# Kernel tuning notes

Hardware: AMD Instinct MI355X
Metric: run time of the kernel (lower is better)

## Reference

```python
import jax, jax.numpy as jnp
import numpy as np

# Sizes: B graphs of N nodes each, K nearest neighbours, D=feat_dim=nhid, C=pos_dim
B, N, K, D, C = 4, 1024, 128, 32, 2
L = 3                     # number of EGNN conv layers
E_IN = 2 * D + 1          # edge MLP input: feats_i | feats_j | rel_dist (edge_dim=0, fourier=0)
E_H = 2 * E_IN            # edge MLP hidden


def _lin(key, fan_in, fan_out):
    kw, kb = jax.random.split(key)
    w = jax.random.normal(kw, (fan_in, fan_out), jnp.float32) / np.sqrt(fan_in)
    b = jax.random.normal(kb, (fan_out,), jnp.float32) * 0.01
    return w, b


def _stack(key, fan_in, fan_out):
    ws, bs = zip(*[_lin(k, fan_in, fan_out) for k in jax.random.split(key, L)])
    return jnp.stack(ws), jnp.stack(bs)


def setup_inputs() -> dict:
    key = jax.random.key(0)
    ks = jax.random.split(key, 10)
    feat_ = jax.random.normal(ks[0], (B * N, D), jnp.float32)
    coor_ = jax.random.normal(ks[1], (B * N, C), jnp.float32)
    batch = jnp.full((B,), N, dtype=jnp.int32)   # per-graph node counts (equal-size graphs)
    embed_w, embed_b = _lin(ks[2], D, D)         # embed: Linear(feat_dim, nhid)
    e1_w, e1_b = _stack(ks[3], E_IN, E_H)        # edge MLP
    e2_w, e2_b = _stack(ks[4], E_H, D)           # -> m_dim = nhid
    gate_w, gate_b = _stack(ks[5], D, 1)         # soft_edges gate
    c1_w, c1_b = _stack(ks[6], D, 4 * D)         # coors MLP
    c2_w, c2_b = _stack(ks[7], 4 * D, 1)
    n1_w, n1_b = _stack(ks[8], 2 * D, 2 * D)     # node MLP
    n2_w, n2_b = _stack(ks[9], 2 * D, D)
    coors_scale = jnp.full((L, 1), 1e-2, jnp.float32)  # CoorsNorm scale (init 1e-2)
    return dict(feat_=feat_, coor_=coor_, batch=batch, embed_w=embed_w, embed_b=embed_b,
                e1_w=e1_w, e1_b=e1_b, e2_w=e2_w, e2_b=e2_b, gate_w=gate_w, gate_b=gate_b,
                c1_w=c1_w, c1_b=c1_b, c2_w=c2_w, c2_b=c2_b, n1_w=n1_w, n1_b=n1_b,
                n2_w=n2_w, n2_b=n2_b, coors_scale=coors_scale)


def _lrelu(x):
    return jax.nn.leaky_relu(x, 0.1)


def _gather(x, idx):
    # x: [B, n, d], idx: [B, n, k] -> [B, n, k, d]
    return jax.vmap(lambda xb, ib: xb[ib])(x, idx)


def _egnn_layer(feats, coors, p):
    (e1_w, e1_b, e2_w, e2_b, gate_w, gate_b, c1_w, c1_b, c2_w, c2_b,
     n1_w, n1_b, n2_w, n2_b, scale) = p
    # pairwise squared distances; k smallest (self included, valid_radius=inf)
    diff = coors[:, :, None, :] - coors[:, None, :, :]      # [B,n,n,C]
    dist = jnp.sum(diff * diff, axis=-1)                    # [B,n,n]
    neg_d, idx = jax.lax.top_k(-dist, K)                    # k nearest
    rel_dist = -neg_d[..., None]                            # [B,n,K,1]
    rel_coors = coors[:, :, None, :] - _gather(coors, idx)  # [B,n,K,C]
    feats_j = _gather(feats, idx)                           # [B,n,K,D]
    feats_i = jnp.broadcast_to(feats[:, :, None, :], feats_j.shape)
    edge_in = jnp.concatenate([feats_i, feats_j, rel_dist], axis=-1)  # [B,n,K,E_IN]
    # edge MLP: Lin -> act -> Lin -> act ; soft edge gate
    m = _lrelu(_lrelu(edge_in @ e1_w + e1_b) @ e2_w + e2_b)            # [B,n,K,D]
    m = m * jax.nn.sigmoid(m @ gate_w + gate_b)
    # coordinate update: coors_mlp -> scalar weights; CoorsNorm on rel coords
    cw = (_lrelu(m @ c1_w + c1_b) @ c2_w + c2_b)[..., 0]               # [B,n,K]
    norm = jnp.maximum(jnp.linalg.norm(rel_coors, axis=-1, keepdims=True), 1e-8)
    rel_n = rel_coors / norm * scale
    coors_out = jnp.einsum('bik,bikc->bic', cw, rel_n) + coors
    # feature update: sum-pool messages, node MLP with residual
    m_i = jnp.sum(m, axis=2)                                           # [B,n,D]
    node_in = jnp.concatenate([feats, m_i], axis=-1)
    feats_out = _lrelu(node_in @ n1_w + n1_b) @ n2_w + n2_b + feats
    return feats_out, coors_out


def reference(feat_, coor_, batch, embed_w, embed_b, e1_w, e1_b, e2_w, e2_b,
              gate_w, gate_b, c1_w, c1_b, c2_w, c2_b, n1_w, n1_b, n2_w, n2_b,
              coors_scale):
    # embed MLP (dropout is identity at p=0 / eval), then batch equal-size graphs
    feats = _lrelu(feat_ @ embed_w + embed_b).reshape(B, N, D)
    coors = coor_.reshape(B, N, C)
    for l in range(L):
        p = (e1_w[l], e1_b[l], e2_w[l], e2_b[l], gate_w[l], gate_b[l],
             c1_w[l], c1_b[l], c2_w[l], c2_b[l], n1_w[l], n1_b[l],
             n2_w[l], n2_b[l], coors_scale[l])
        feats, coors = _egnn_layer(feats, coors, p)
    return feats.reshape(B * N, D)
```

## Files before the change

### kernel.cpp

```cpp
#include <hip/hip_runtime.h>
#include <hip/hip_bf16.h>
#include <math.h>

#define BB 4
#define NN 1024
#define KK 128
#define DD 32
#define LL 3
#define EH 130

typedef float f32x4 __attribute__((ext_vector_type(4)));
typedef short s16x8 __attribute__((ext_vector_type(8)));

__device__ __forceinline__ float lrelu(float x) { return fmaxf(x, 0.1f * x); }

__device__ __forceinline__ unsigned pk2(float a, float b) {
    __hip_bfloat162 h = __float22bfloat162_rn(float2{a, b});
    return *(unsigned*)&h;
}
__device__ __forceinline__ unsigned short bf16_hu(float v) {
    return (unsigned short)((__float_as_uint(v) + 0x8000u) >> 16);
}
__device__ __forceinline__ unsigned short bf16_rne(float v) {
    unsigned u = __float_as_uint(v);
    return (unsigned short)((u + 0x7fffu + ((u >> 16) & 1u)) >> 16);
}
__device__ __forceinline__ float bf2f(unsigned short h) {
    return __uint_as_float(((unsigned)h) << 16);
}

__device__ __forceinline__ void knn_block(const float2* __restrict__ cbp, int i, int t,
                                          unsigned* __restrict__ hist,
                                          volatile unsigned* __restrict__ scr,
                                          int* __restrict__ nb) {
    const int lane = t & 63, wid = t >> 6;
    unsigned* histw = hist + wid * 256;
    const float2 ci = cbp[i];
    unsigned k[4];
#pragma unroll
    for (int s = 0; s < 4; s++) {
        float2 cj = cbp[wid * 256 + s * 64 + lane];
        float dx = ci.x - cj.x, dy = ci.y - cj.y;
        float d = __fadd_rn(__fmul_rn(dx, dx), __fmul_rn(dy, dy));
        k[s] = __float_as_uint(d);
    }
    unsigned prefix = 0u;
    unsigned r = KK - 1;
#pragma unroll
    for (int pass = 0; pass < 4; pass++) {
        const int sh = 24 - 8 * pass;
        const unsigned mpref = (pass == 0) ? 0u : (0xFFFFFFFFu << (sh + 8));
        ((uint4*)histw)[lane] = uint4{0u, 0u, 0u, 0u};
#pragma unroll
        for (int s = 0; s < 4; s++) {
            if ((k[s] & mpref) == prefix)
                atomicAdd(&histw[(k[s] >> sh) & 255u], 1u);
        }
        __syncthreads();
        unsigned tot = hist[t] + hist[256 + t] + hist[512 + t] + hist[768 + t];
        unsigned incl = tot;
#pragma unroll
        for (int off = 1; off < 64; off <<= 1) {
            unsigned v = __shfl_up(incl, off, 64);
            if (lane >= off) incl += v;
        }
        if (lane == 63) scr[wid] = incl;
        __syncthreads();
        unsigned woff = 0;
#pragma unroll
        for (int w = 0; w < 4; w++)
            if (w < wid) woff += scr[w];
        incl += woff;
        const unsigned excl = incl - tot;
        if (r >= excl && r < incl) { scr[4] = (unsigned)t; scr[5] = r - excl; }
        __syncthreads();
        prefix |= scr[4] << sh;
        r = scr[5];
    }
    const unsigned dstar = prefix;

    const unsigned long long below = (1ull << lane) - 1ull;
    unsigned long long mL[4], mE[4];
    unsigned cntL = 0, cntE = 0;
#pragma unroll
    for (int s = 0; s < 4; s++) {
        mL[s] = __ballot(k[s] < dstar);
        mE[s] = __ballot(k[s] == dstar);
        cntL += (unsigned)__popcll(mL[s]);
        cntE += (unsigned)__popcll(mE[s]);
    }
    if (lane == 0) { scr[8 + wid] = cntL; scr[12 + wid] = cntE; }
    __syncthreads();
    unsigned offL = 0, offE = 0, totalL = 0;
#pragma unroll
    for (int w = 0; w < 4; w++) {
        unsigned cl = scr[8 + w];
        if (w < wid) { offL += cl; offE += scr[12 + w]; }
        totalL += cl;
    }
    unsigned run = offL;
#pragma unroll
    for (int s = 0; s < 4; s++) {
        if (k[s] < dstar) nb[run + (unsigned)__popcll(mL[s] & below)] = wid * 256 + s * 64 + lane;
        run += (unsigned)__popcll(mL[s]);
    }
    const int need = KK - (int)totalL;
    unsigned tie = offE;
#pragma unroll
    for (int s = 0; s < 4; s++) {
        if (k[s] == dstar) {
            unsigned r2 = tie + (unsigned)__popcll(mE[s] & below);
            if ((int)r2 < need) nb[totalL + r2] = wid * 256 + s * 64 + lane;
        }
        tie += (unsigned)__popcll(mE[s]);
    }
}

__global__ __launch_bounds__(128) void prep_kernel(
    const float* __restrict__ feat,
    const float* __restrict__ ew, const float* __restrict__ eb,
    float* __restrict__ fout, unsigned short* __restrict__ fouth, unsigned short* __restrict__ foutl,
    const float* __restrict__ e1w,
    const float* __restrict__ e2w, const float* __restrict__ e2b,
    const float* __restrict__ c1w,
    unsigned short* __restrict__ e2f, unsigned short* __restrict__ c1f,
    unsigned short* __restrict__ e1Jh, unsigned short* __restrict__ e1Jl) {
    const int bid = blockIdx.x;
    const int t = threadIdx.x;
    if (bid < 2048) {
        const int n0 = bid * 2;
        if (t < 64) {
            const int nl = t >> 5, o = t & 31;
            const float* f = feat + (size_t)(n0 + nl) * DD;
            float a = eb[o];
#pragma unroll
            for (int k = 0; k < DD; k++) a = fmaf(f[k], ew[k * DD + o], a);
            a = lrelu(a);
            const size_t off = (size_t)(n0 + nl) * DD + o;
            fout[off] = a;
            const unsigned short h = bf16_rne(a);
            fouth[off] = h;
            foutl[off] = bf16_rne(a - bf2f(h));
        }
    } else {
        const int A_ = LL * 5120;
        const int B_ = A_ + LL * 4096;
        const int C_ = B_ + LL * 4608;
        const int TOT = C_ + LL * 4608;
        for (int u = (bid - 2048) * 128 + t; u < TOT; u += 432 * 128) {
            if (u < A_) {
                int l = u / 5120, v = u - l * 5120;
                int jj = v & 7, la = (v >> 3) & 63, nt = (v >> 9) & 1, c = v >> 10;
                int n = nt * 16 + (la & 15);
                float val;
                if (c < 4) {
                    int k = 32 * c + (la >> 4) * 8 + jj;
                    val = e2w[(size_t)l * EH * DD + k * DD + n];
                } else {
                    int ks = (la >> 4) * 8 + jj;
                    val = (ks == 0) ? e2w[((size_t)l * EH + 128) * DD + n]
                        : (ks == 1) ? e2w[((size_t)l * EH + 129) * DD + n]
                        : (ks == 2) ? e2b[(size_t)l * DD + n] : 0.f;
                }
                e2f[u] = bf16_rne(val);
            } else if (u < B_) {
                int v = u - A_;
                int jj = v & 7, la = (v >> 3) & 63, nt = (v >> 9) & 7, l = v >> 12;
                int k = (la >> 4) * 8 + jj;
                int n = nt * 16 + (la & 15);
                c1f[v] = bf16_rne(c1w[(size_t)l * DD * 128 + k * 128 + n]);
            } else {
                const int isLo = (u >= C_);
                int v = u - (isLo ? C_ : B_);
                int l = v / 4608, w = v - l * 4608;
                int jj = w & 7, la = (w >> 3) & 63, nt = w >> 9;
                int col = nt * 16 + (la & 15);
                int k = (la >> 4) * 8 + jj;
                float val = (col < EH) ? e1w[(size_t)l * 65 * EH + (size_t)(DD + k) * EH + col] : 0.f;
                const unsigned short h = bf16_rne(val);
                if (!isLo) e1Jh[v] = h;
                else       e1Jl[v] = bf16_rne(val - bf2f(h));
            }
        }
    }
}

__global__ __launch_bounds__(256) void layer_kernel(
    const float* __restrict__ feats_in,
    const unsigned short* __restrict__ finh, const unsigned short* __restrict__ finl,
    const float* __restrict__ coors_in,
    const float* __restrict__ e1wI,
    const float* __restrict__ e1b_l,
    const float* __restrict__ w65,
    const unsigned short* __restrict__ e2f,
    const unsigned short* __restrict__ c1f,
    const unsigned short* __restrict__ e1Jh, const unsigned short* __restrict__ e1Jl,
    const float* __restrict__ gw, const float* __restrict__ gb,
    const float* __restrict__ c1b, const float* __restrict__ c2w, const float* __restrict__ c2b,
    const float* __restrict__ n1w, const float* __restrict__ n1b,
    const float* __restrict__ n2w, const float* __restrict__ n2b,
    const float* __restrict__ scale,
    float* __restrict__ feats_out,
    unsigned short* __restrict__ fouth, unsigned short* __restrict__ foutl,
    float* __restrict__ coors_out) {
    const int node = blockIdx.x;
    const int b = node >> 10;
    const int t = threadIdx.x;
    const int lane = t & 63, wid = t >> 6;
    const int ln = lane & 15, q = lane >> 4;
    const int rowbase = wid * 32;

    __shared__ __align__(16) float shi[144];
    __shared__ __align__(16) float sw65[144];
    __shared__ __align__(16) unsigned short smA[4 * 32 * 32];
    __shared__ unsigned sknn[16];
    __shared__ float sx0[128], sx1[128], su[128], sv[128], srd[128];
    __shared__ int snb[128];
    __shared__ float sgw[DD], sfi[DD];
    __shared__ float sc1b[128], sc2w[128];
    __shared__ float redm[4][DD], redc[4][2];
    __shared__ float sni[2 * DD], shd[2 * DD];
    __shared__ float sp1[4][2 * DD], sp2[4][DD];

    for (int u = t; u < 144; u += 256) sw65[u] = (u < EH) ? w65[u] : 0.f;
    if (t < DD) { sfi[t] = feats_in[node * DD + t]; sgw[t] = gw[t]; }
    if (t >= 128 && t < 256) { sc1b[t - 128] = c1b[t - 128]; sc2w[t - 128] = c2w[t - 128]; }
    __syncthreads();

    if (t < EH) {
        float a = e1b_l[t];
#pragma unroll
        for (int k = 0; k < DD; k++) a = fmaf(sfi[k], e1wI[k * EH + t], a);
        shi[t] = a;
    } else if (t < 144) {
        shi[t] = 0.f;
    }

    knn_block((const float2*)coors_in + (size_t)b * NN, node & (NN - 1), t,
              (unsigned*)smA, sknn, snb);
    __syncthreads();

    const float cix = coors_in[node * 2], ciy = coors_in[node * 2 + 1];
    if (t < 128) {
        const int j = snb[t];
        const float2 cj = *(const float2*)(coors_in + ((size_t)(b * NN) + j) * 2);
        const float dx = cix - cj.x, dy = ciy - cj.y;
        const float rd = __fadd_rn(__fmul_rn(dx, dx), __fmul_rn(dy, dy));
        srd[t] = rd;
        const float nrm = fmaxf(sqrtf(rd), 1e-8f);
        const float s = scale[0] / nrm;
        su[t] = dx * s;
        sv[t] = dy * s;
    }
    __syncthreads();

    s16x8 ah[2], al[2];
    float rd8[2][4];
#pragma unroll
    for (int mt = 0; mt < 2; mt++) {
        const int row = rowbase + mt * 16 + ln;
        const size_t jb = ((size_t)(b * NN) + snb[row]) * DD;
        ah[mt] = *(const s16x8*)(finh + jb + q * 8);
        al[mt] = *(const s16x8*)(finl + jb + q * 8);
#pragma unroll
        for (int r = 0; r < 4; r++) rd8[mt][r] = srd[rowbase + mt * 16 + q * 4 + r];
    }

    const f32x4 zz = {0.f, 0.f, 0.f, 0.f};
    f32x4 accA[2][2];
    accA[0][0] = zz; accA[0][1] = zz; accA[1][0] = zz; accA[1][1] = zz;
    unsigned short* smw = smA + wid * (32 * 32);

#pragma unroll 1
    for (int c = 0; c < 4; c++) {
        s16x8 bh0 = *(const s16x8*)(e1Jh + ((c * 2 + 0) * 64 + lane) * 8);
        s16x8 bl0 = *(const s16x8*)(e1Jl + ((c * 2 + 0) * 64 + lane) * 8);
        s16x8 bh1 = *(const s16x8*)(e1Jh + ((c * 2 + 1) * 64 + lane) * 8);
        s16x8 bl1 = *(const s16x8*)(e1Jl + ((c * 2 + 1) * 64 + lane) * 8);
        const float h0 = shi[c * 32 + ln],      h1 = shi[c * 32 + 16 + ln];
        const float w0 = sw65[c * 32 + ln],     w1 = sw65[c * 32 + 16 + ln];
        const f32x4 ci0 = {h0, h0, h0, h0};
        const f32x4 ci1 = {h1, h1, h1, h1};
#pragma unroll
        for (int mt = 0; mt < 2; mt++) {
            f32x4 s0 = __builtin_amdgcn_mfma_f32_16x16x32_bf16(ah[mt], bh0, ci0, 0, 0, 0);
            s0 = __builtin_amdgcn_mfma_f32_16x16x32_bf16(ah[mt], bl0, s0, 0, 0, 0);
            s0 = __builtin_amdgcn_mfma_f32_16x16x32_bf16(al[mt], bh0, s0, 0, 0, 0);
            f32x4 s1 = __builtin_amdgcn_mfma_f32_16x16x32_bf16(ah[mt], bh1, ci1, 0, 0, 0);
            s1 = __builtin_amdgcn_mfma_f32_16x16x32_bf16(ah[mt], bl1, s1, 0, 0, 0);
            s1 = __builtin_amdgcn_mfma_f32_16x16x32_bf16(al[mt], bh1, s1, 0, 0, 0);
#pragma unroll
            for (int r = 0; r < 4; r++) {
                const float x0 = lrelu(fmaf(rd8[mt][r], w0, s0[r]));
                const float x1 = lrelu(fmaf(rd8[mt][r], w1, s1[r]));
                const int prow = (r << 3) | (4 * mt + q);
                smw[prow * 32 + ln] = bf16_hu(x0);
                smw[prow * 32 + 16 + ln] = bf16_hu(x1);
            }
        }
        s16x8 b0 = *(const s16x8*)(e2f + ((c * 2 + 0) * 64 + lane) * 8);
        s16x8 b1 = *(const s16x8*)(e2f + ((c * 2 + 1) * 64 + lane) * 8);
#pragma unroll
        for (int mt = 0; mt < 2; mt++) {
            const int prow = ((ln & 3) << 3) | (4 * mt + (ln >> 2));
            s16x8 a4x = *(const s16x8*)(smw + prow * 32 + q * 8);
            accA[mt][0] = __builtin_amdgcn_mfma_f32_16x16x32_bf16(a4x, b0, accA[mt][0], 0, 0, 0);
            accA[mt][1] = __builtin_amdgcn_mfma_f32_16x16x32_bf16(a4x, b1, accA[mt][1], 0, 0, 0);
        }
    }

    {
        s16x8 bh8 = *(const s16x8*)(e1Jh + (8 * 64 + lane) * 8);
        s16x8 bl8 = *(const s16x8*)(e1Jl + (8 * 64 + lane) * 8);
        const float h8 = shi[128 + ln];
        const float w8 = sw65[128 + ln];
        const f32x4 ci8 = {h8, h8, h8, h8};
#pragma unroll
        for (int mt = 0; mt < 2; mt++) {
            f32x4 s = __builtin_amdgcn_mfma_f32_16x16x32_bf16(ah[mt], bh8, ci8, 0, 0, 0);
            s = __builtin_amdgcn_mfma_f32_16x16x32_bf16(ah[mt], bl8, s, 0, 0, 0);
            s = __builtin_amdgcn_mfma_f32_16x16x32_bf16(al[mt], bh8, s, 0, 0, 0);
#pragma unroll
            for (int r = 0; r < 4; r++) {
                const float v = lrelu(fmaf(rd8[mt][r], w8, s[r]));
                const int row = rowbase + mt * 16 + q * 4 + r;
                if (ln == 0) sx0[row] = v;
                else if (ln == 1) sx1[row] = v;
            }
        }
    }

    {
        s16x8 b40 = *(const s16x8*)(e2f + (8 * 64 + lane) * 8);
        s16x8 b41 = *(const s16x8*)(e2f + (9 * 64 + lane) * 8);
#pragma unroll
        for (int mt = 0; mt < 2; mt++) {
            const int row = rowbase + mt * 16 + ln;
            union { s16x8 v; unsigned u[4]; } A;
            const unsigned p0 = pk2(sx0[row], sx1[row]);
            A.u[0] = (q == 0) ? p0 : 0u;
            A.u[1] = (q == 0) ? 0x00003f80u : 0u;
            A.u[2] = 0u;
            A.u[3] = 0u;
            accA[mt][0] = __builtin_amdgcn_mfma_f32_16x16x32_bf16(A.v, b40, accA[mt][0], 0, 0, 0);
            accA[mt][1] = __builtin_amdgcn_mfma_f32_16x16x32_bf16(A.v, b41, accA[mt][1], 0, 0, 0);
        }
    }

    s16x8 cfr[8];
#pragma unroll
    for (int g8 = 0; g8 < 8; g8++)
        cfr[g8] = *(const s16x8*)(c1f + (g8 * 64 + lane) * 8);

#pragma unroll
    for (int mt = 0; mt < 2; mt++)
#pragma unroll
        for (int nt = 0; nt < 2; nt++)
#pragma unroll
            for (int r = 0; r < 4; r++)
                accA[mt][nt][r] = lrelu(accA[mt][nt][r]);

    const float gbv = gb[0];
#pragma unroll
    for (int mt = 0; mt < 2; mt++) {
        float p[4];
#pragma unroll
        for (int r = 0; r < 4; r++)
            p[r] = accA[mt][0][r] * sgw[ln] + accA[mt][1][r] * sgw[16 + ln];
#pragma unroll
        for (int off = 1; off <= 8; off <<= 1)
#pragma unroll
            for (int r = 0; r < 4; r++) p[r] += __shfl_xor(p[r], off);
#pragma unroll
        for (int r = 0; r < 4; r++) {
            const float g = 1.f / (1.f + __expf(-(p[r] + gbv)));
            accA[mt][0][r] *= g;
            accA[mt][1][r] *= g;
        }
    }

    float mi0 = 0.f, mi1 = 0.f;
#pragma unroll
    for (int mt = 0; mt < 2; mt++)
#pragma unroll
        for (int r = 0; r < 4; r++) { mi0 += accA[mt][0][r]; mi1 += accA[mt][1][r]; }
    mi0 += __shfl_xor(mi0, 16); mi0 += __shfl_xor(mi0, 32);
    mi1 += __shfl_xor(mi1, 16); mi1 += __shfl_xor(mi1, 32);
    if (lane < 16) { redm[wid][lane] = mi0; redm[wid][16 + lane] = mi1; }

#pragma unroll
    for (int mt = 0; mt < 2; mt++)
#pragma unroll
        for (int nt = 0; nt < 2; nt++)
#pragma unroll
            for (int r = 0; r < 4; r++) {
                const int prow = (r << 3) | (4 * mt + q);
                smw[prow * 32 + nt * 16 + ln] = bf16_hu(accA[mt][nt][r]);
            }

    s16x8 a4[2];
#pragma unroll
    for (int mt = 0; mt < 2; mt++) {
        const int prow = ((ln & 3) << 3) | (4 * mt + (ln >> 2));
        a4[mt] = *(const s16x8*)(smw + prow * 32 + q * 8);
    }

    float cacc[2][4];
#pragma unroll
    for (int mt = 0; mt < 2; mt++)
#pragma unroll
        for (int r = 0; r < 4; r++) cacc[mt][r] = 0.f;

#pragma unroll
    for (int g = 0; g < 4; g++) {
        const float cb0 = sc1b[(2 * g + 0) * 16 + ln];
        const float cb1 = sc1b[(2 * g + 1) * 16 + ln];
        const f32x4 ci0 = {cb0, cb0, cb0, cb0};
        const f32x4 ci1 = {cb1, cb1, cb1, cb1};
        f32x4 c20[2], c21[2];
#pragma unroll
        for (int mt = 0; mt < 2; mt++) {
            c20[mt] = __builtin_amdgcn_mfma_f32_16x16x32_bf16(a4[mt], cfr[2 * g + 0], ci0, 0, 0, 0);
            c21[mt] = __builtin_amdgcn_mfma_f32_16x16x32_bf16(a4[mt], cfr[2 * g + 1], ci1, 0, 0, 0);
        }
#pragma unroll
        for (int h = 0; h < 2; h++) {
            const float c2wv = sc2w[(2 * g + h) * 16 + ln];
#pragma unroll
            for (int mt = 0; mt < 2; mt++)
#pragma unroll
                for (int r = 0; r < 4; r++) {
                    const float v = (h ? c21[mt][r] : c20[mt][r]);
                    cacc[mt][r] = fmaf(lrelu(v), c2wv, cacc[mt][r]);
                }
        }
    }
#pragma unroll
    for (int off = 1; off <= 8; off <<= 1)
#pragma unroll
        for (int mt = 0; mt < 2; mt++)
#pragma unroll
            for (int r = 0; r < 4; r++) cacc[mt][r] += __shfl_xor(cacc[mt][r], off);

    const float c2bv = c2b[0];
    float vxp = 0.f, vyp = 0.f;
    if (ln == 0) {
#pragma unroll
        for (int mt = 0; mt < 2; mt++)
#pragma unroll
            for (int r = 0; r < 4; r++) {
                const int row = rowbase + mt * 16 + q * 4 + r;
                const float cw = cacc[mt][r] + c2bv;
                vxp = fmaf(cw, su[row], vxp);
                vyp = fmaf(cw, sv[row], vyp);
            }
    }
    vxp += __shfl_xor(vxp, 16); vxp += __shfl_xor(vxp, 32);
    vyp += __shfl_xor(vyp, 16); vyp += __shfl_xor(vyp, 32);
    if (lane == 0) { redc[wid][0] = vxp; redc[wid][1] = vyp; }

    __syncthreads();
    if (t < DD) {
        sni[t] = sfi[t];
        sni[DD + t] = redm[0][t] + redm[1][t] + redm[2][t] + redm[3][t];
    }
    __syncthreads();
    {
        const int o = t & 63, p = t >> 6;
        float a = 0.f;
#pragma unroll
        for (int k = 0; k < 16; k++) a = fmaf(sni[p * 16 + k], n1w[(p * 16 + k) * 64 + o], a);
        sp1[p][o] = a;
    }
    __syncthreads();
    if (t < 2 * DD)
        shd[t] = lrelu(n1b[t] + ((sp1[0][t] + sp1[1][t]) + (sp1[2][t] + sp1[3][t])));
    __syncthreads();
    if (t < 128) {
        const int o = t & 31, p = t >> 5;
        float a = 0.f;
#pragma unroll
        for (int k = 0; k < 16; k++) a = fmaf(shd[p * 16 + k], n2w[(p * 16 + k) * DD + o], a);
        sp2[p][o] = a;
    }
    __syncthreads();
    if (t < DD) {
        const float val = n2b[t] + ((sp2[0][t] + sp2[1][t]) + (sp2[2][t] + sp2[3][t])) + sfi[t];
        feats_out[node * DD + t] = val;
        if (fouth) {
            const unsigned short h = bf16_rne(val);
            fouth[node * DD + t] = h;
            foutl[node * DD + t] = bf16_rne(val - bf2f(h));
        }
    }
    if (t == 0) {
        coors_out[node * 2]     = cix + redc[0][0] + redc[1][0] + redc[2][0] + redc[3][0];
        coors_out[node * 2 + 1] = ciy + redc[0][1] + redc[1][1] + redc[2][1] + redc[3][1];
    }
}

extern "C" void kernel_launch(void* const* d_in, const int* in_sizes, int n_in,
                              void* d_out, int out_size, void* d_ws, size_t ws_size,
                              hipStream_t stream) {
    const float* feat_   = (const float*)d_in[0];
    const float* coor_   = (const float*)d_in[1];
    const float* embed_w = (const float*)d_in[3];
    const float* embed_b = (const float*)d_in[4];
    const float* e1_w    = (const float*)d_in[5];
    const float* e1_b    = (const float*)d_in[6];
    const float* e2_w    = (const float*)d_in[7];
    const float* e2_b    = (const float*)d_in[8];
    const float* gate_w  = (const float*)d_in[9];
    const float* gate_b  = (const float*)d_in[10];
    const float* c1_w    = (const float*)d_in[11];
    const float* c1_b    = (const float*)d_in[12];
    const float* c2_w    = (const float*)d_in[13];
    const float* c2_b    = (const float*)d_in[14];
    const float* n1_w    = (const float*)d_in[15];
    const float* n1_b    = (const float*)d_in[16];
    const float* n2_w    = (const float*)d_in[17];
    const float* n2_b    = (const float*)d_in[18];
    const float* cscale  = (const float*)d_in[19];

    float* ws = (float*)d_ws;
    float* fa   = ws;   ws += BB * NN * DD;
    float* fb   = ws;   ws += BB * NN * DD;
    float* ca   = ws;   ws += BB * NN * 2;
    float* cb2  = ws;   ws += BB * NN * 2;
    unsigned short* e2f  = (unsigned short*)ws;
    unsigned short* c1f  = e2f + LL * 5120;
    unsigned short* e1Jh = c1f + LL * 4096;
    unsigned short* e1Jl = e1Jh + LL * 4608;
    unsigned short* fah  = e1Jl + LL * 4608;
    unsigned short* fal  = fah + BB * NN * DD;
    unsigned short* fbh  = fal + BB * NN * DD;
    unsigned short* fbl  = fbh + BB * NN * DD;

    prep_kernel<<<2048 + 432, 128, 0, stream>>>(feat_, embed_w, embed_b,
                                                fa, fah, fal,
                                                e1_w, e2_w, e2_b, c1_w,
                                                e2f, c1f, e1Jh, e1Jl);

    const float* fin = fa;
    const unsigned short* finh = fah;
    const unsigned short* finl = fal;
    const float* cin = coor_;
    float* fouts[LL]          = {fb, fa, (float*)d_out};
    unsigned short* fouth[LL] = {fbh, fah, nullptr};
    unsigned short* foutl[LL] = {fbl, fal, nullptr};
    float* couts[LL] = {ca, cb2, ca};

    for (int l = 0; l < LL; l++) {
        layer_kernel<<<BB * NN, 256, 0, stream>>>(
            fin, finh, finl, cin,
            e1_w + (size_t)l * 65 * EH,
            e1_b + (size_t)l * EH,
            e1_w + ((size_t)l * 65 + 64) * EH,
            e2f + (size_t)l * 5120,
            c1f + (size_t)l * 4096,
            e1Jh + (size_t)l * 4608,
            e1Jl + (size_t)l * 4608,
            gate_w + (size_t)l * DD,
            gate_b + l,
            c1_b + (size_t)l * 128,
            c2_w + (size_t)l * 128,
            c2_b + l,
            n1_w + (size_t)l * 64 * 64,
            n1_b + (size_t)l * 64,
            n2_w + (size_t)l * 64 * 32,
            n2_b + (size_t)l * DD,
            cscale + l,
            fouts[l], fouth[l], foutl[l],
            couts[l]);
        fin = fouts[l];
        finh = fouth[l];
        finl = foutl[l];
        cin = couts[l];
    }
}
```

Before: 322.4 us.

## Process two nodes per block with joint radix-select kNN

```diff
diff --git a/kernel.cpp b/kernel.cpp
--- a/kernel.cpp
+++ b/kernel.cpp
@@ -8,6 +8,7 @@
 #define DD 32
 #define LL 3
 #define EH 130
+#define SMS 40
 
 typedef float f32x4 __attribute__((ext_vector_type(4)));
 typedef short s16x8 __attribute__((ext_vector_type(8)));
@@ -29,91 +30,111 @@
     return __uint_as_float(((unsigned)h) << 16);
 }
 
-__device__ __forceinline__ void knn_block(const float2* __restrict__ cbp, int i, int t,
-                                          unsigned* __restrict__ hist,
-                                          volatile unsigned* __restrict__ scr,
-                                          int* __restrict__ nb) {
+__device__ __forceinline__ void knn2_block(const float2* __restrict__ cbp, int iA, int iB,
+                                           int t,
+                                           unsigned* __restrict__ hist,
+                                           volatile unsigned* __restrict__ scr,
+                                           int* __restrict__ nbA, int* __restrict__ nbB) {
     const int lane = t & 63, wid = t >> 6;
-    unsigned* histw = hist + wid * 256;
-    const float2 ci = cbp[i];
-    unsigned k[4];
+    unsigned* hA = hist + wid * 256;
+    unsigned* hB = hist + 1024 + wid * 256;
+    const float2 cA = cbp[iA], cB = cbp[iB];
+    unsigned kA[4], kB[4];
 #pragma unroll
     for (int s = 0; s < 4; s++) {
         float2 cj = cbp[wid * 256 + s * 64 + lane];
-        float dx = ci.x - cj.x, dy = ci.y - cj.y;
-        float d = __fadd_rn(__fmul_rn(dx, dx), __fmul_rn(dy, dy));
-        k[s] = __float_as_uint(d);
-    }
-    unsigned prefix = 0u;
-    unsigned r = KK - 1;
+        float dxA = cA.x - cj.x, dyA = cA.y - cj.y;
+        kA[s] = __float_as_uint(__fadd_rn(__fmul_rn(dxA, dxA), __fmul_rn(dyA, dyA)));
+        float dxB = cB.x - cj.x, dyB = cB.y - cj.y;
+        kB[s] = __float_as_uint(__fadd_rn(__fmul_rn(dxB, dxB), __fmul_rn(dyB, dyB)));
+    }
+    unsigned prefA = 0u, rA = KK - 1, prefB = 0u, rB = KK - 1;
 #pragma unroll
     for (int pass = 0; pass < 4; pass++) {
         const int sh = 24 - 8 * pass;
         const unsigned mpref = (pass == 0) ? 0u : (0xFFFFFFFFu << (sh + 8));
-        ((uint4*)histw)[lane] = uint4{0u, 0u, 0u, 0u};
+        ((uint4*)hA)[lane] = uint4{0u, 0u, 0u, 0u};
+        ((uint4*)hB)[lane] = uint4{0u, 0u, 0u, 0u};
 #pragma unroll
         for (int s = 0; s < 4; s++) {
-            if ((k[s] & mpref) == prefix)
-                atomicAdd(&histw[(k[s] >> sh) & 255u], 1u);
-        }
-        __syncthreads();
-        unsigned tot = hist[t] + hist[256 + t] + hist[512 + t] + hist[768 + t];
-        unsigned incl = tot;
+            if ((kA[s] & mpref) == prefA) atomicAdd(&hA[(kA[s] >> sh) & 255u], 1u);
+            if ((kB[s] & mpref) == prefB) atomicAdd(&hB[(kB[s] >> sh) & 255u], 1u);
+        }
+        __syncthreads();
+        unsigned totA = hist[t] + hist[256 + t] + hist[512 + t] + hist[768 + t];
+        unsigned totB = hist[1024 + t] + hist[1280 + t] + hist[1536 + t] + hist[1792 + t];
+        unsigned inA = totA, inB = totB;
 #pragma unroll
         for (int off = 1; off < 64; off <<= 1) {
-            unsigned v = __shfl_up(incl, off, 64);
-            if (lane >= off) incl += v;
-        }
-        if (lane == 63) scr[wid] = incl;
-        __syncthreads();
-        unsigned woff = 0;
+            unsigned vA = __shfl_up(inA, off, 64);
+            unsigned vB = __shfl_up(inB, off, 64);
+            if (lane >= off) { inA += vA; inB += vB; }
+        }
+        if (lane == 63) { scr[wid] = inA; scr[4 + wid] = inB; }
+        __syncthreads();
+        unsigned woA = 0, woB = 0;
 #pragma unroll
         for (int w = 0; w < 4; w++)
-            if (w < wid) woff += scr[w];
-        incl += woff;
-        const unsigned excl = incl - tot;
-        if (r >= excl && r < incl) { scr[4] = (unsigned)t; scr[5] = r - excl; }
-        __syncthreads();
-        prefix |= scr[4] << sh;
-        r = scr[5];
-    }
-    const unsigned dstar = prefix;
+            if (w < wid) { woA += scr[w]; woB += scr[4 + w]; }
+        inA += woA; inB += woB;
+        const unsigned exA = inA - totA, exB = inB - totB;
+        if (rA >= exA && rA < inA) { scr[8] = (unsigned)t; scr[9] = rA - exA; }
+        if (rB >= exB && rB < inB) { scr[10] = (unsigned)t; scr[11] = rB - exB; }
+        __syncthreads();
+        prefA |= scr[8] << sh;   rA = scr[9];
+        prefB |= scr[10] << sh;  rB = scr[11];
+    }
+    const unsigned dsA = prefA, dsB = prefB;
 
     const unsigned long long below = (1ull << lane) - 1ull;
-    unsigned long long mL[4], mE[4];
-    unsigned cntL = 0, cntE = 0;
+    unsigned long long mLA[4], mEA[4], mLB[4], mEB[4];
+    unsigned cLA = 0, cEA = 0, cLB = 0, cEB = 0;
 #pragma unroll
     for (int s = 0; s < 4; s++) {
-        mL[s] = __ballot(k[s] < dstar);
-        mE[s] = __ballot(k[s] == dstar);
-        cntL += (unsigned)__popcll(mL[s]);
-        cntE += (unsigned)__popcll(mE[s]);
-    }
-    if (lane == 0) { scr[8 + wid] = cntL; scr[12 + wid] = cntE; }
+        mLA[s] = __ballot(kA[s] < dsA);   mEA[s] = __ballot(kA[s] == dsA);
+        cLA += (unsigned)__popcll(mLA[s]); cEA += (unsigned)__popcll(mEA[s]);
+        mLB[s] = __ballot(kB[s] < dsB);   mEB[s] = __ballot(kB[s] == dsB);
+        cLB += (unsigned)__popcll(mLB[s]); cEB += (unsigned)__popcll(mEB[s]);
+    }
+    if (lane == 0) {
+        scr[12 + wid] = cLA; scr[16 + wid] = cEA;
+        scr[20 + wid] = cLB; scr[24 + wid] = cEB;
+    }
     __syncthreads();
-    unsigned offL = 0, offE = 0, totalL = 0;
+    unsigned offLA = 0, offEA = 0, totLA = 0;
+    unsigned offLB = 0, offEB = 0, totLB = 0;
 #pragma unroll
     for (int w = 0; w < 4; w++) {
-        unsigned cl = scr[8 + w];
-        if (w < wid) { offL += cl; offE += scr[12 + w]; }
-        totalL += cl;
-    }
-    unsigned run = offL;
+        unsigned a = scr[12 + w], bb2 = scr[20 + w];
+        if (w < wid) { offLA += a; offEA += scr[16 + w]; offLB += bb2; offEB += scr[24 + w]; }
+        totLA += a; totLB += bb2;
+    }
+    unsigned runA = offLA, runB = offLB;
 #pragma unroll
     for (int s = 0; s < 4; s++) {
-        if (k[s] < dstar) nb[run + (unsigned)__popcll(mL[s] & below)] = wid * 256 + s * 64 + lane;
-        run += (unsigned)__popcll(mL[s]);
-    }
-    const int need = KK - (int)totalL;
-    unsigned tie = offE;
+        const int cand = wid * 256 + s * 64 + lane;
+        if (kA[s] < dsA) nbA[runA + (unsigned)__popcll(mLA[s] & below)] = cand;
+        runA += (unsigned)__popcll(mLA[s]);
+        if (kB[s] < dsB) nbB[runB + (unsigned)__popcll(mLB[s] & below)] = cand;
+        runB += (unsigned)__popcll(mLB[s]);
+    }
+    const int needA = KK - (int)totLA, needB = KK - (int)totLB;
+    unsigned tieA = offEA, tieB = offEB;
 #pragma unroll
     for (int s = 0; s < 4; s++) {
-        if (k[s] == dstar) {
-            unsigned r2 = tie + (unsigned)__popcll(mE[s] & below);
-            if ((int)r2 < need) nb[totalL + r2] = wid * 256 + s * 64 + lane;
-        }
-        tie += (unsigned)__popcll(mE[s]);
-    }
+        const int cand = wid * 256 + s * 64 + lane;
+        if (kA[s] == dsA) {
+            unsigned r2 = tieA + (unsigned)__popcll(mEA[s] & below);
+            if ((int)r2 < needA) nbA[totLA + r2] = cand;
+        }
+        tieA += (unsigned)__popcll(mEA[s]);
+        if (kB[s] == dsB) {
+            unsigned r2 = tieB + (unsigned)__popcll(mEB[s] & below);
+            if ((int)r2 < needB) nbB[totLB + r2] = cand;
+        }
+        tieB += (unsigned)__popcll(mEB[s]);
+    }
+    __syncthreads();
 }
 
 __global__ __launch_bounds__(128) void prep_kernel(
@@ -203,8 +224,8 @@
     float* __restrict__ feats_out,
     unsigned short* __restrict__ fouth, unsigned short* __restrict__ foutl,
     float* __restrict__ coors_out) {
-    const int node = blockIdx.x;
-    const int b = node >> 10;
+    const int node0 = blockIdx.x * 2;
+    const int b = node0 >> 10;
     const int t = threadIdx.x;
     const int lane = t & 63, wid = t >> 6;
     const int ln = lane & 15, q = lane >> 4;
@@ -212,10 +233,10 @@
 
     __shared__ __align__(16) float shi[144];
     __shared__ __align__(16) float sw65[144];
-    __shared__ __align__(16) unsigned short smA[4 * 32 * 32];
-    __shared__ unsigned sknn[16];
+    __shared__ __align__(16) unsigned short smA[4 * 32 * SMS];
+    __shared__ unsigned sknn[32];
     __shared__ float sx0[128], sx1[128], su[128], sv[128], srd[128];
-    __shared__ int snb[128];
+    __shared__ int snb[2 * 128];
     __shared__ float sgw[DD], sfi[DD];
     __shared__ float sc1b[128], sc2w[128];
     __shared__ float redm[4][DD], redc[4][2];
@@ -223,279 +244,287 @@
     __shared__ float sp1[4][2 * DD], sp2[4][DD];
 
     for (int u = t; u < 144; u += 256) sw65[u] = (u < EH) ? w65[u] : 0.f;
-    if (t < DD) { sfi[t] = feats_in[node * DD + t]; sgw[t] = gw[t]; }
-    if (t >= 128 && t < 256) { sc1b[t - 128] = c1b[t - 128]; sc2w[t - 128] = c2w[t - 128]; }
-    __syncthreads();
-
-    if (t < EH) {
-        float a = e1b_l[t];
-#pragma unroll
-        for (int k = 0; k < DD; k++) a = fmaf(sfi[k], e1wI[k * EH + t], a);
-        shi[t] = a;
-    } else if (t < 144) {
-        shi[t] = 0.f;
-    }
-
-    knn_block((const float2*)coors_in + (size_t)b * NN, node & (NN - 1), t,
-              (unsigned*)smA, sknn, snb);
-    __syncthreads();
-
-    const float cix = coors_in[node * 2], ciy = coors_in[node * 2 + 1];
-    if (t < 128) {
-        const int j = snb[t];
-        const float2 cj = *(const float2*)(coors_in + ((size_t)(b * NN) + j) * 2);
-        const float dx = cix - cj.x, dy = ciy - cj.y;
-        const float rd = __fadd_rn(__fmul_rn(dx, dx), __fmul_rn(dy, dy));
-        srd[t] = rd;
-        const float nrm = fmaxf(sqrtf(rd), 1e-8f);
-        const float s = scale[0] / nrm;
-        su[t] = dx * s;
-        sv[t] = dy * s;
-    }
-    __syncthreads();
-
-    s16x8 ah[2], al[2];
-    float rd8[2][4];
-#pragma unroll
-    for (int mt = 0; mt < 2; mt++) {
-        const int row = rowbase + mt * 16 + ln;
-        const size_t jb = ((size_t)(b * NN) + snb[row]) * DD;
-        ah[mt] = *(const s16x8*)(finh + jb + q * 8);
-        al[mt] = *(const s16x8*)(finl + jb + q * 8);
-#pragma unroll
-        for (int r = 0; r < 4; r++) rd8[mt][r] = srd[rowbase + mt * 16 + q * 4 + r];
-    }
-
+    if (t < DD) sgw[t] = gw[t];
+    if (t >= 128) { sc1b[t - 128] = c1b[t - 128]; sc2w[t - 128] = c2w[t - 128]; }
+
+    knn2_block((const float2*)coors_in + (size_t)b * NN, node0 & (NN - 1),
+               (node0 & (NN - 1)) + 1, t, (unsigned*)smA, sknn, snb, snb + 128);
+
+    unsigned short* smw = smA + wid * (32 * SMS);
     const f32x4 zz = {0.f, 0.f, 0.f, 0.f};
-    f32x4 accA[2][2];
-    accA[0][0] = zz; accA[0][1] = zz; accA[1][0] = zz; accA[1][1] = zz;
-    unsigned short* smw = smA + wid * (32 * 32);
 
 #pragma unroll 1
-    for (int c = 0; c < 4; c++) {
-        s16x8 bh0 = *(const s16x8*)(e1Jh + ((c * 2 + 0) * 64 + lane) * 8);
-        s16x8 bl0 = *(const s16x8*)(e1Jl + ((c * 2 + 0) * 64 + lane) * 8);
-        s16x8 bh1 = *(const s16x8*)(e1Jh + ((c * 2 + 1) * 64 + lane) * 8);
-        s16x8 bl1 = *(const s16x8*)(e1Jl + ((c * 2 + 1) * 64 + lane) * 8);
-        const float h0 = shi[c * 32 + ln],      h1 = shi[c * 32 + 16 + ln];
-        const float w0 = sw65[c * 32 + ln],     w1 = sw65[c * 32 + 16 + ln];
-        const f32x4 ci0 = {h0, h0, h0, h0};
-        const f32x4 ci1 = {h1, h1, h1, h1};
+    for (int nn = 0; nn < 2; nn++) {
+        const int node = node0 + nn;
+        const int* snbn = snb + nn * 128;
+
+        __syncthreads();
+        if (t < DD) sfi[t] = feats_in[node * DD + t];
+        __syncthreads();
+
+        const float cix = coors_in[node * 2], ciy = coors_in[node * 2 + 1];
+        if (t < EH) {
+            float a = e1b_l[t];
+#pragma unroll
+            for (int k = 0; k < DD; k++) a = fmaf(sfi[k], e1wI[k * EH + t], a);
+            shi[t] = a;
+        } else if (t < 144) {
+            shi[t] = 0.f;
+        }
+        if (t < 128) {
+            const int j = snbn[t];
+            const float2 cj = *(const float2*)(coors_in + ((size_t)(b * NN) + j) * 2);
+            const float dx = cix - cj.x, dy = ciy - cj.y;
+            const float rd = __fadd_rn(__fmul_rn(dx, dx), __fmul_rn(dy, dy));
+            srd[t] = rd;
+            const float nrm = fmaxf(sqrtf(rd), 1e-8f);
+            const float s = scale[0] / nrm;
+            su[t] = dx * s;
+            sv[t] = dy * s;
+        }
+        __syncthreads();
+
+        s16x8 ah[2], al[2];
+        float rd8[2][4];
 #pragma unroll
         for (int mt = 0; mt < 2; mt++) {
-            f32x4 s0 = __builtin_amdgcn_mfma_f32_16x16x32_bf16(ah[mt], bh0, ci0, 0, 0, 0);
-            s0 = __builtin_amdgcn_mfma_f32_16x16x32_bf16(ah[mt], bl0, s0, 0, 0, 0);
-            s0 = __builtin_amdgcn_mfma_f32_16x16x32_bf16(al[mt], bh0, s0, 0, 0, 0);
-            f32x4 s1 = __builtin_amdgcn_mfma_f32_16x16x32_bf16(ah[mt], bh1, ci1, 0, 0, 0);
-            s1 = __builtin_amdgcn_mfma_f32_16x16x32_bf16(ah[mt], bl1, s1, 0, 0, 0);
-            s1 = __builtin_amdgcn_mfma_f32_16x16x32_bf16(al[mt], bh1, s1, 0, 0, 0);
+            const int row = rowbase + mt * 16 + ln;
+            const size_t jb = ((size_t)(b * NN) + snbn[row]) * DD;
+            ah[mt] = *(const s16x8*)(finh + jb + q * 8);
+            al[mt] = *(const s16x8*)(finl + jb + q * 8);
+#pragma unroll
+            for (int r = 0; r < 4; r++) rd8[mt][r] = srd[rowbase + mt * 16 + q * 4 + r];
+        }
+
+        f32x4 accA[2][2];
+        accA[0][0] = zz; accA[0][1] = zz; accA[1][0] = zz; accA[1][1] = zz;
+
+#pragma unroll 1
+        for (int c = 0; c < 4; c++) {
+            s16x8 bh0 = *(const s16x8*)(e1Jh + ((c * 2 + 0) * 64 + lane) * 8);
+            s16x8 bl0 = *(const s16x8*)(e1Jl + ((c * 2 + 0) * 64 + lane) * 8);
+            s16x8 bh1 = *(const s16x8*)(e1Jh + ((c * 2 + 1) * 64 + lane) * 8);
+            s16x8 bl1 = *(const s16x8*)(e1Jl + ((c * 2 + 1) * 64 + lane) * 8);
+            const float h0 = shi[c * 32 + ln],      h1 = shi[c * 32 + 16 + ln];
+            const float w0 = sw65[c * 32 + ln],     w1 = sw65[c * 32 + 16 + ln];
+            const f32x4 ci0 = {h0, h0, h0, h0};
+            const f32x4 ci1 = {h1, h1, h1, h1};
+#pragma unroll
+            for (int mt = 0; mt < 2; mt++) {
+                f32x4 s0 = __builtin_amdgcn_mfma_f32_16x16x32_bf16(ah[mt], bh0, ci0, 0, 0, 0);
+                s0 = __builtin_amdgcn_mfma_f32_16x16x32_bf16(ah[mt], bl0, s0, 0, 0, 0);
+                s0 = __builtin_amdgcn_mfma_f32_16x16x32_bf16(al[mt], bh0, s0, 0, 0, 0);
+                f32x4 s1 = __builtin_amdgcn_mfma_f32_16x16x32_bf16(ah[mt], bh1, ci1, 0, 0, 0);
+                s1 = __builtin_amdgcn_mfma_f32_16x16x32_bf16(ah[mt], bl1, s1, 0, 0, 0);
+                s1 = __builtin_amdgcn_mfma_f32_16x16x32_bf16(al[mt], bh1, s1, 0, 0, 0);
+#pragma unroll
+                for (int r = 0; r < 4; r++) {
+                    const float x0 = lrelu(fmaf(rd8[mt][r], w0, s0[r]));
+                    const float x1 = lrelu(fmaf(rd8[mt][r], w1, s1[r]));
+                    const int prow = (r << 3) | (4 * mt + q);
+                    smw[prow * SMS + ln] = bf16_hu(x0);
+                    smw[prow * SMS + 16 + ln] = bf16_hu(x1);
+                }
+            }
+            s16x8 b0 = *(const s16x8*)(e2f + ((c * 2 + 0) * 64 + lane) * 8);
+            s16x8 b1 = *(const s16x8*)(e2f + ((c * 2 + 1) * 64 + lane) * 8);
+#pragma unroll
+            for (int mt = 0; mt < 2; mt++) {
+                const int prow = ((ln & 3) << 3) | (4 * mt + (ln >> 2));
+                s16x8 a4x = *(const s16x8*)(smw + prow * SMS + q * 8);
+                accA[mt][0] = __builtin_amdgcn_mfma_f32_16x16x32_bf16(a4x, b0, accA[mt][0], 0, 0, 0);
+                accA[mt][1] = __builtin_amdgcn_mfma_f32_16x16x32_bf16(a4x, b1, accA[mt][1], 0, 0, 0);
+            }
+        }
+
+        {
+            s16x8 bh8 = *(const s16x8*)(e1Jh + (8 * 64 + lane) * 8);
+            s16x8 bl8 = *(const s16x8*)(e1Jl + (8 * 64 + lane) * 8);
+            const float h8 = shi[128 + ln];
+            const float w8 = sw65[128 + ln];
+            const f32x4 ci8 = {h8, h8, h8, h8};
+#pragma unroll
+            for (int mt = 0; mt < 2; mt++) {
+                f32x4 s = __builtin_amdgcn_mfma_f32_16x16x32_bf16(ah[mt], bh8, ci8, 0, 0, 0);
+                s = __builtin_amdgcn_mfma_f32_16x16x32_bf16(ah[mt], bl8, s, 0, 0, 0);
+                s = __builtin_amdgcn_mfma_f32_16x16x32_bf16(al[mt], bh8, s, 0, 0, 0);
+#pragma unroll
+                for (int r = 0; r < 4; r++) {
+                    const float v = lrelu(fmaf(rd8[mt][r], w8, s[r]));
+                    const int row = rowbase + mt * 16 + q * 4 + r;
+                    if (ln == 0) sx0[row] = v;
+                    else if (ln == 1) sx1[row] = v;
+                }
+            }
+        }
+
+        {
+            s16x8 b40 = *(const s16x8*)(e2f + (8 * 64 + lane) * 8);
+            s16x8 b41 = *(const s16x8*)(e2f + (9 * 64 + lane) * 8);
+#pragma unroll
+            for (int mt = 0; mt < 2; mt++) {
+                const int row = rowbase + mt * 16 + ln;
+                union { s16x8 v; unsigned u[4]; } A;
+                const unsigned p0 = pk2(sx0[row], sx1[row]);
+                A.u[0] = (q == 0) ? p0 : 0u;
+                A.u[1] = (q == 0) ? 0x00003f80u : 0u;
+                A.u[2] = 0u;
+                A.u[3] = 0u;
+                accA[mt][0] = __builtin_amdgcn_mfma_f32_16x16x32_bf16(A.v, b40, accA[mt][0], 0, 0, 0);
+                accA[mt][1] = __builtin_amdgcn_mfma_f32_16x16x32_bf16(A.v, b41, accA[mt][1], 0, 0, 0);
+            }
+        }
+
+        s16x8 cfr[8];
+#pragma unroll
+        for (int g8 = 0; g8 < 8; g8++)
+            cfr[g8] = *(const s16x8*)(c1f + (g8 * 64 + lane) * 8);
+
+#pragma unroll
+        for (int mt = 0; mt < 2; mt++)
+#pragma unroll
+            for (int nt = 0; nt < 2; nt++)
+#pragma unroll
+                for (int r = 0; r < 4; r++)
+                    accA[mt][nt][r] = lrelu(accA[mt][nt][r]);
+
+        const float gbv = gb[0];
+#pragma unroll
+        for (int mt = 0; mt < 2; mt++) {
+            float p[4];
+#pragma unroll
+            for (int r = 0; r < 4; r++)
+                p[r] = accA[mt][0][r] * sgw[ln] + accA[mt][1][r] * sgw[16 + ln];
+#pragma unroll
+            for (int off = 1; off <= 8; off <<= 1)
+#pragma unroll
+                for (int r = 0; r < 4; r++) p[r] += __shfl_xor(p[r], off);
 #pragma unroll
             for (int r = 0; r < 4; r++) {
-                const float x0 = lrelu(fmaf(rd8[mt][r], w0, s0[r]));
-                const float x1 = lrelu(fmaf(rd8[mt][r], w1, s1[r]));
-                const int prow = (r << 3) | (4 * mt + q);
-                smw[prow * 32 + ln] = bf16_hu(x0);
-                smw[prow * 32 + 16 + ln] = bf16_hu(x1);
-            }
-        }
-        s16x8 b0 = *(const s16x8*)(e2f + ((c * 2 + 0) * 64 + lane) * 8);
-        s16x8 b1 = *(const s16x8*)(e2f + ((c * 2 + 1) * 64 + lane) * 8);
+                const float g = 1.f / (1.f + __expf(-(p[r] + gbv)));
+                accA[mt][0][r] *= g;
+                accA[mt][1][r] *= g;
+            }
+        }
+
+        float mi0 = 0.f, mi1 = 0.f;
+#pragma unroll
+        for (int mt = 0; mt < 2; mt++)
+#pragma unroll
+            for (int r = 0; r < 4; r++) { mi0 += accA[mt][0][r]; mi1 += accA[mt][1][r]; }
+        mi0 += __shfl_xor(mi0, 16); mi0 += __shfl_xor(mi0, 32);
+        mi1 += __shfl_xor(mi1, 16); mi1 += __shfl_xor(mi1, 32);
+        if (lane < 16) { redm[wid][lane] = mi0; redm[wid][16 + lane] = mi1; }
+
+#pragma unroll
+        for (int mt = 0; mt < 2; mt++)
+#pragma unroll
+            for (int nt = 0; nt < 2; nt++)
+#pragma unroll
+                for (int r = 0; r < 4; r++) {
+                    const int prow = (r << 3) | (4 * mt + q);
+                    smw[prow * SMS + nt * 16 + ln] = bf16_hu(accA[mt][nt][r]);
+                }
+
+        s16x8 a4[2];
 #pragma unroll
         for (int mt = 0; mt < 2; mt++) {
             const int prow = ((ln & 3) << 3) | (4 * mt + (ln >> 2));
-            s16x8 a4x = *(const s16x8*)(smw + prow * 32 + q * 8);
-            accA[mt][0] = __builtin_amdgcn_mfma_f32_16x16x32_bf16(a4x, b0, accA[mt][0], 0, 0, 0);
-            accA[mt][1] = __builtin_amdgcn_mfma_f32_16x16x32_bf16(a4x, b1, accA[mt][1], 0, 0, 0);
-        }
-    }
-
-    {
-        s16x8 bh8 = *(const s16x8*)(e1Jh + (8 * 64 + lane) * 8);
-        s16x8 bl8 = *(const s16x8*)(e1Jl + (8 * 64 + lane) * 8);
-        const float h8 = shi[128 + ln];
-        const float w8 = sw65[128 + ln];
-        const f32x4 ci8 = {h8, h8, h8, h8};
-#pragma unroll
-        for (int mt = 0; mt < 2; mt++) {
-            f32x4 s = __builtin_amdgcn_mfma_f32_16x16x32_bf16(ah[mt], bh8, ci8, 0, 0, 0);
-            s = __builtin_amdgcn_mfma_f32_16x16x32_bf16(ah[mt], bl8, s, 0, 0, 0);
-            s = __builtin_amdgcn_mfma_f32_16x16x32_bf16(al[mt], bh8, s, 0, 0, 0);
-#pragma unroll
-            for (int r = 0; r < 4; r++) {
-                const float v = lrelu(fmaf(rd8[mt][r], w8, s[r]));
-                const int row = rowbase + mt * 16 + q * 4 + r;
-                if (ln == 0) sx0[row] = v;
-                else if (ln == 1) sx1[row] = v;
-            }
-        }
-    }
-
-    {
-        s16x8 b40 = *(const s16x8*)(e2f + (8 * 64 + lane) * 8);
-        s16x8 b41 = *(const s16x8*)(e2f + (9 * 64 + lane) * 8);
-#pragma unroll
-        for (int mt = 0; mt < 2; mt++) {
-            const int row = rowbase + mt * 16 + ln;
-            union { s16x8 v; unsigned u[4]; } A;
-            const unsigned p0 = pk2(sx0[row], sx1[row]);
-            A.u[0] = (q == 0) ? p0 : 0u;
-            A.u[1] = (q == 0) ? 0x00003f80u : 0u;
-            A.u[2] = 0u;
-            A.u[3] = 0u;
-            accA[mt][0] = __builtin_amdgcn_mfma_f32_16x16x32_bf16(A.v, b40, accA[mt][0], 0, 0, 0);
-            accA[mt][1] = __builtin_amdgcn_mfma_f32_16x16x32_bf16(A.v, b41, accA[mt][1], 0, 0, 0);
-        }
-    }
-
-    s16x8 cfr[8];
-#pragma unroll
-    for (int g8 = 0; g8 < 8; g8++)
-        cfr[g8] = *(const s16x8*)(c1f + (g8 * 64 + lane) * 8);
-
-#pragma unroll
-    for (int mt = 0; mt < 2; mt++)
-#pragma unroll
-        for (int nt = 0; nt < 2; nt++)
-#pragma unroll
-            for (int r = 0; r < 4; r++)
-                accA[mt][nt][r] = lrelu(accA[mt][nt][r]);
-
-    const float gbv = gb[0];
-#pragma unroll
-    for (int mt = 0; mt < 2; mt++) {
-        float p[4];
-#pragma unroll
-        for (int r = 0; r < 4; r++)
-            p[r] = accA[mt][0][r] * sgw[ln] + accA[mt][1][r] * sgw[16 + ln];
+            a4[mt] = *(const s16x8*)(smw + prow * SMS + q * 8);
+        }
+
+        float cacc[2][4];
+#pragma unroll
+        for (int mt = 0; mt < 2; mt++)
+#pragma unroll
+            for (int r = 0; r < 4; r++) cacc[mt][r] = 0.f;
+
+#pragma unroll
+        for (int g = 0; g < 4; g++) {
+            const float cb0 = sc1b[(2 * g + 0) * 16 + ln];
+            const float cb1 = sc1b[(2 * g + 1) * 16 + ln];
+            const f32x4 ci0 = {cb0, cb0, cb0, cb0};
+            const f32x4 ci1 = {cb1, cb1, cb1, cb1};
+            f32x4 c20[2], c21[2];
+#pragma unroll
+            for (int mt = 0; mt < 2; mt++) {
+                c20[mt] = __builtin_amdgcn_mfma_f32_16x16x32_bf16(a4[mt], cfr[2 * g + 0], ci0, 0, 0, 0);
+                c21[mt] = __builtin_amdgcn_mfma_f32_16x16x32_bf16(a4[mt], cfr[2 * g + 1], ci1, 0, 0, 0);
+            }
+#pragma unroll
+            for (int h = 0; h < 2; h++) {
+                const float c2wv = sc2w[(2 * g + h) * 16 + ln];
+#pragma unroll
+                for (int mt = 0; mt < 2; mt++)
+#pragma unroll
+                    for (int r = 0; r < 4; r++) {
+                        const float v = (h ? c21[mt][r] : c20[mt][r]);
+                        cacc[mt][r] = fmaf(lrelu(v), c2wv, cacc[mt][r]);
+                    }
+            }
+        }
 #pragma unroll
         for (int off = 1; off <= 8; off <<= 1)
 #pragma unroll
-            for (int r = 0; r < 4; r++) p[r] += __shfl_xor(p[r], off);
-#pragma unroll
-        for (int r = 0; r < 4; r++) {
-            const float g = 1.f / (1.f + __expf(-(p[r] + gbv)));
-            accA[mt][0][r] *= g;
-            accA[mt][1][r] *= g;
-        }
-    }
-
-    float mi0 = 0.f, mi1 = 0.f;
-#pragma unroll
-    for (int mt = 0; mt < 2; mt++)
-#pragma unroll
-        for (int r = 0; r < 4; r++) { mi0 += accA[mt][0][r]; mi1 += accA[mt][1][r]; }
-    mi0 += __shfl_xor(mi0, 16); mi0 += __shfl_xor(mi0, 32);
-    mi1 += __shfl_xor(mi1, 16); mi1 += __shfl_xor(mi1, 32);
-    if (lane < 16) { redm[wid][lane] = mi0; redm[wid][16 + lane] = mi1; }
-
-#pragma unroll
-    for (int mt = 0; mt < 2; mt++)
-#pragma unroll
-        for (int nt = 0; nt < 2; nt++)
-#pragma unroll
-            for (int r = 0; r < 4; r++) {
-                const int prow = (r << 3) | (4 * mt + q);
-                smw[prow * 32 + nt * 16 + ln] = bf16_hu(accA[mt][nt][r]);
-            }
-
-    s16x8 a4[2];
-#pragma unroll
-    for (int mt = 0; mt < 2; mt++) {
-        const int prow = ((ln & 3) << 3) | (4 * mt + (ln >> 2));
-        a4[mt] = *(const s16x8*)(smw + prow * 32 + q * 8);
-    }
-
-    float cacc[2][4];
-#pragma unroll
-    for (int mt = 0; mt < 2; mt++)
-#pragma unroll
-        for (int r = 0; r < 4; r++) cacc[mt][r] = 0.f;
-
-#pragma unroll
-    for (int g = 0; g < 4; g++) {
-        const float cb0 = sc1b[(2 * g + 0) * 16 + ln];
-        const float cb1 = sc1b[(2 * g + 1) * 16 + ln];
-        const f32x4 ci0 = {cb0, cb0, cb0, cb0};
-        const f32x4 ci1 = {cb1, cb1, cb1, cb1};
-        f32x4 c20[2], c21[2];
-#pragma unroll
-        for (int mt = 0; mt < 2; mt++) {
-            c20[mt] = __builtin_amdgcn_mfma_f32_16x16x32_bf16(a4[mt], cfr[2 * g + 0], ci0, 0, 0, 0);
-            c21[mt] = __builtin_amdgcn_mfma_f32_16x16x32_bf16(a4[mt], cfr[2 * g + 1], ci1, 0, 0, 0);
-        }
-#pragma unroll
-        for (int h = 0; h < 2; h++) {
-            const float c2wv = sc2w[(2 * g + h) * 16 + ln];
-#pragma unroll
             for (int mt = 0; mt < 2; mt++)
 #pragma unroll
+                for (int r = 0; r < 4; r++) cacc[mt][r] += __shfl_xor(cacc[mt][r], off);
+
+        const float c2bv = c2b[0];
+        float vxp = 0.f, vyp = 0.f;
+        if (ln == 0) {
+#pragma unroll
+            for (int mt = 0; mt < 2; mt++)
+#pragma unroll
                 for (int r = 0; r < 4; r++) {
-                    const float v = (h ? c21[mt][r] : c20[mt][r]);
-                    cacc[mt][r] = fmaf(lrelu(v), c2wv, cacc[mt][r]);
+                    const int row = rowbase + mt * 16 + q * 4 + r;
+                    const float cw = cacc[mt][r] + c2bv;
+                    vxp = fmaf(cw, su[row], vxp);
+                    vyp = fmaf(cw, sv[row], vyp);
                 }
         }
-    }
-#pragma unroll
-    for (int off = 1; off <= 8; off <<= 1)
-#pragma unroll
-        for (int mt = 0; mt < 2; mt++)
-#pragma unroll
-            for (int r = 0; r < 4; r++) cacc[mt][r] += __shfl_xor(cacc[mt][r], off);
-
-    const float c2bv = c2b[0];
-    float vxp = 0.f, vyp = 0.f;
-    if (ln == 0) {
-#pragma unroll
-        for (int mt = 0; mt < 2; mt++)
-#pragma unroll
-            for (int r = 0; r < 4; r++) {
-                const int row = rowbase + mt * 16 + q * 4 + r;
-                const float cw = cacc[mt][r] + c2bv;
-                vxp = fmaf(cw, su[row], vxp);
-                vyp = fmaf(cw, sv[row], vyp);
-            }
-    }
-    vxp += __shfl_xor(vxp, 16); vxp += __shfl_xor(vxp, 32);
-    vyp += __shfl_xor(vyp, 16); vyp += __shfl_xor(vyp, 32);
-    if (lane == 0) { redc[wid][0] = vxp; redc[wid][1] = vyp; }
-
-    __syncthreads();
-    if (t < DD) {
-        sni[t] = sfi[t];
-        sni[DD + t] = redm[0][t] + redm[1][t] + redm[2][t] + redm[3][t];
-    }
-    __syncthreads();
-    {
-        const int o = t & 63, p = t >> 6;
-        float a = 0.f;
-#pragma unroll
-        for (int k = 0; k < 16; k++) a = fmaf(sni[p * 16 + k], n1w[(p * 16 + k) * 64 + o], a);
-        sp1[p][o] = a;
-    }
-    __syncthreads();
-    if (t < 2 * DD)
-        shd[t] = lrelu(n1b[t] + ((sp1[0][t] + sp1[1][t]) + (sp1[2][t] + sp1[3][t])));
-    __syncthreads();
-    if (t < 128) {
-        const int o = t & 31, p = t >> 5;
-        float a = 0.f;
-#pragma unroll
-        for (int k = 0; k < 16; k++) a = fmaf(shd[p * 16 + k], n2w[(p * 16 + k) * DD + o], a);
-        sp2[p][o] = a;
-    }
-    __syncthreads();
-    if (t < DD) {
-        const float val = n2b[t] + ((sp2[0][t] + sp2[1][t]) + (sp2[2][t] + sp2[3][t])) + sfi[t];
-        feats_out[node * DD + t] = val;
-        if (fouth) {
-            const unsigned short h = bf16_rne(val);
-            fouth[node * DD + t] = h;
-            foutl[node * DD + t] = bf16_rne(val - bf2f(h));
-        }
-    }
-    if (t == 0) {
-        coors_out[node * 2]     = cix + redc[0][0] + redc[1][0] + redc[2][0] + redc[3][0];
-        coors_out[node * 2 + 1] = ciy + redc[0][1] + redc[1][1] + redc[2][1] + redc[3][1];
+        vxp += __shfl_xor(vxp, 16); vxp += __shfl_xor(vxp, 32);
+        vyp += __shfl_xor(vyp, 16); vyp += __shfl_xor(vyp, 32);
+        if (lane == 0) { redc[wid][0] = vxp; redc[wid][1] = vyp; }
+
+        __syncthreads();
+        if (t < DD) {
+            sni[t] = sfi[t];
+            sni[DD + t] = redm[0][t] + redm[1][t] + redm[2][t] + redm[3][t];
+        }
+        __syncthreads();
+        {
+            const int o = t & 63, p = t >> 6;
+            float a = 0.f;
+#pragma unroll
+            for (int k = 0; k < 16; k++) a = fmaf(sni[p * 16 + k], n1w[(p * 16 + k) * 64 + o], a);
+            sp1[p][o] = a;
+        }
+        __syncthreads();
+        if (t < 2 * DD)
+            shd[t] = lrelu(n1b[t] + ((sp1[0][t] + sp1[1][t]) + (sp1[2][t] + sp1[3][t])));
+        __syncthreads();
+        if (t < 128) {
+            const int o = t & 31, p = t >> 5;
+            float a = 0.f;
+#pragma unroll
+            for (int k = 0; k < 16; k++) a = fmaf(shd[p * 16 + k], n2w[(p * 16 + k) * DD + o], a);
+            sp2[p][o] = a;
+        }
+        __syncthreads();
+        if (t < DD) {
+            const float val = n2b[t] + ((sp2[0][t] + sp2[1][t]) + (sp2[2][t] + sp2[3][t])) + sfi[t];
+            feats_out[node * DD + t] = val;
+            if (fouth) {
+                const unsigned short h = bf16_rne(val);
+                fouth[node * DD + t] = h;
+                foutl[node * DD + t] = bf16_rne(val - bf2f(h));
+            }
+        }
+        if (t == 0) {
+            coors_out[node * 2]     = cix + redc[0][0] + redc[1][0] + redc[2][0] + redc[3][0];
+            coors_out[node * 2 + 1] = ciy + redc[0][1] + redc[1][1] + redc[2][1] + redc[3][1];
+        }
     }
 }
 
@@ -551,7 +580,7 @@
     float* couts[LL] = {ca, cb2, ca};
 
     for (int l = 0; l < LL; l++) {
-        layer_kernel<<<BB * NN, 256, 0, stream>>>(
+        layer_kernel<<<BB * NN / 2, 256, 0, stream>>>(
             fin, finh, finl, cin,
             e1_w + (size_t)l * 65 * EH,
             e1_b + (size_t)l * EH,
```

Result: slower. 771.0 us (+139.2%).
